# Kernel tuning notes

Measured on AMD Instinct MI355X. Metric: run time of the kernel, lower is better.

## Reference

```python
import jax, jax.numpy as jnp
import numpy as np
from jax.scipy.special import logsumexp

B, T, V, E, H, C, L = 128, 1024, 21, 32, 100, 20, 2


def setup_inputs() -> dict:
    key = jax.random.key(0)
    ks = jax.random.split(key, 32)
    def n(i, shape, scale=0.1):
        return (jax.random.normal(ks[i], shape) * scale).astype(jnp.float32)
    inp = {}
    inp["tokens"] = jax.random.randint(ks[0], (B, T), 0, V)
    inp["seq_lengths"] = jnp.full((B,), T, dtype=jnp.int32)
    inp["emb"] = n(1, (V, E), 1.0)
    idx = 2
    for l in range(L):
        din = E if l == 0 else 2 * H
        for sfx in ["", "_rev"]:
            inp[f"W_ih_l{l}{sfx}"] = n(idx, (4 * H, din)); idx += 1
            inp[f"W_hh_l{l}{sfx}"] = n(idx, (4 * H, H)); idx += 1
            inp[f"b_ih_l{l}{sfx}"] = n(idx, (4 * H,)); idx += 1
            inp[f"b_hh_l{l}{sfx}"] = n(idx, (4 * H,)); idx += 1
    inp["fW"] = n(idx, (C, 2 * H)); idx += 1
    inp["fb"] = n(idx, (C,)); idx += 1
    inp["gW"] = n(idx, (C * C, 2 * H)); idx += 1
    inp["gb"] = n(idx, (C * C,)); idx += 1
    inp["h0"] = n(idx, (2 * L, B, H), 1.0); idx += 1
    inp["c0"] = n(idx, (2 * L, B, H), 1.0)
    return inp


def _lstm_dir(x, Wih, Whh, bih, bhh, h0, c0, reverse):
    # x: [B,T,D]; precompute input projection once (PyTorch gate order i,f,g,o)
    xp = jnp.einsum('btd,gd->btg', x, Wih) + bih + bhh  # [B,T,4H]
    def step(carry, xt):
        h, c = carry
        gates = xt + h @ Whh.T
        i, f, g, o = jnp.split(gates, 4, axis=-1)
        c = jax.nn.sigmoid(f) * c + jax.nn.sigmoid(i) * jnp.tanh(g)
        h = jax.nn.sigmoid(o) * jnp.tanh(c)
        return (h, c), h
    _, hs = jax.lax.scan(step, (h0, c0), jnp.swapaxes(xp, 0, 1), reverse=reverse)
    return jnp.swapaxes(hs, 0, 1)  # [B,T,H]


def _crf_alpha(f, g):
    # alpha[0]=f[0]; alpha[t]=f[t]+LSE_i(alpha[t-1,i]+g[t,i,:])
    fs = jnp.swapaxes(f, 0, 1)  # [T,B,C]
    gs = jnp.swapaxes(g, 0, 1)  # [T,B,C,C]
    def step(a, fg):
        ft, gt = fg
        a = ft + logsumexp(a[:, :, None] + gt, axis=1)
        return a, a
    _, alphas = jax.lax.scan(step, fs[0], (fs[1:], gs[1:]))
    return jnp.swapaxes(jnp.concatenate([fs[:1], alphas], 0), 0, 1)


def _crf_beta(f, g):
    # beta[T-1]=0; beta[t]=LSE_j(g[t+1,:,j]+f[t+1,j]+beta[t+1,j])
    fs = jnp.swapaxes(f, 0, 1)
    gs = jnp.swapaxes(g, 0, 1)
    def step(b, fg):
        fnx, gnx = fg
        b = logsumexp(gnx + (fnx + b)[:, None, :], axis=2)
        return b, b
    bT = jnp.zeros_like(fs[0])
    _, betas = jax.lax.scan(step, bT, (fs[1:], gs[1:]), reverse=True)
    return jnp.swapaxes(jnp.concatenate([betas, bT[None]], 0), 0, 1)


def reference(tokens, seq_lengths, emb,
              W_ih_l0, W_hh_l0, b_ih_l0, b_hh_l0,
              W_ih_l0_rev, W_hh_l0_rev, b_ih_l0_rev, b_hh_l0_rev,
              W_ih_l1, W_hh_l1, b_ih_l1, b_hh_l1,
              W_ih_l1_rev, W_hh_l1_rev, b_ih_l1_rev, b_hh_l1_rev,
              fW, fb, gW, gb, h0, c0):
    x = emb[tokens]  # [B,T,E]
    # layer 0 (bidirectional)
    of = _lstm_dir(x, W_ih_l0, W_hh_l0, b_ih_l0, b_hh_l0, h0[0], c0[0], False)
    ob = _lstm_dir(x, W_ih_l0_rev, W_hh_l0_rev, b_ih_l0_rev, b_hh_l0_rev, h0[1], c0[1], True)
    x1 = jnp.concatenate([of, ob], axis=-1)  # dropout between layers: eval mode (identity)
    # layer 1
    of = _lstm_dir(x1, W_ih_l1, W_hh_l1, b_ih_l1, b_hh_l1, h0[2], c0[2], False)
    ob = _lstm_dir(x1, W_ih_l1_rev, W_hh_l1_rev, b_ih_l1_rev, b_hh_l1_rev, h0[3], c0[3], True)
    h = jnp.concatenate([of, ob], axis=-1)  # [B,T,2H]
    # pad_packed_sequence zeroes positions beyond seq_lengths
    mask = (jnp.arange(T)[None, :] < seq_lengths[:, None]).astype(h.dtype)
    h = h * mask[:, :, None]
    f_out = h @ fW.T + fb                      # [B,T,C] emissions
    g_out = (h @ gW.T + gb).reshape(B, T, C, C)  # [B,T,C,C] transitions
    alpha = _crf_alpha(f_out, g_out)
    beta = _crf_beta(f_out, g_out)
    logZ = logsumexp(alpha[:, -1], axis=-1)    # [B]
    log_marg = alpha + beta - logZ[:, None, None]
    return (jnp.exp(log_marg), f_out, g_out, alpha, beta)
```

## Files before the change

kernel.cpp:

```cpp
#include <hip/hip_runtime.h>
#include <hip/hip_bf16.h>

#define B_ 128
#define T_ 1024
#define E_ 32
#define H_ 100
#define C_ 20
#define M_ (B_*T_)

typedef __attribute__((ext_vector_type(8))) short bf16x8v;
typedef __attribute__((ext_vector_type(4))) float f32x4v;
typedef __attribute__((ext_vector_type(2))) _Float16 h2v;
typedef unsigned short u16;
typedef unsigned int u32;

static __device__ __forceinline__ short f2b(float x) {
  union { __hip_bfloat16 b; short s; } u;
  u.b = __float2bfloat16(x);
  return u.s;
}
static __device__ __forceinline__ float b2f(u16 x) {
  return __uint_as_float(((u32)x) << 16);
}

#if __has_builtin(__builtin_amdgcn_fdot2)
#define FDOT2(w, p, c) __builtin_amdgcn_fdot2((w), (p), (c), false)
#else
static __device__ __forceinline__ float FDOT2(h2v w, h2v p, float c) {
  return fmaf((float)w[1], (float)p[1], fmaf((float)w[0], (float)p[0], c));
}
#endif

__global__ void embed_k(const int* __restrict__ tok, const float* __restrict__ emb,
                        float* __restrict__ x0) {
  int idx = blockIdx.x * 256 + threadIdx.x;
  int bt = idx >> 5;
  int e  = idx & 31;
  x0[idx] = emb[tok[bt] * E_ + e];
}

template<int ABF, int OBF>
__global__ __launch_bounds__(256) void gemm_mfma_t(
    const void* __restrict__ Av, const float* __restrict__ W,
    const float* __restrict__ b1, const float* __restrict__ b2,
    void* __restrict__ Cv, int K, int N, int ldc)
{
  __shared__ short as[64 * 40];
  __shared__ short ws[64 * 40];
  const float* Af = (const float*)Av;
  const u16*   Ab = (const u16*)Av;
  float* Cf = (float*)Cv;
  u16*   Cb = (u16*)Cv;
  int tid = threadIdx.x, lane = tid & 63, w = tid >> 6;
  int lr = lane & 15, lq = lane >> 4;
  size_t m0 = (size_t)blockIdx.x * 64;
  int n0 = blockIdx.y * 64;
  int srow = tid >> 2;
  int sk = (tid & 3) * 8;
  bool wok = (n0 + srow) < N;
  const float* Wp = wok ? (W + (size_t)(n0 + srow) * K + sk) : W;
  size_t arow = (m0 + srow) * (size_t)K;
  f32x4v acc[4];
  #pragma unroll
  for (int r = 0; r < 4; ++r) acc[r] = (f32x4v){0.f, 0.f, 0.f, 0.f};
  int ksteps = (K + 31) / 32;
  for (int ks = 0; ks < ksteps; ++ks) {
    int kk = ks * 32;
    bf16x8v av, wv;
    if (kk + sk + 7 < K) {
      if (ABF) {
        av = *(const bf16x8v*)(Ab + arow + kk + sk);
      } else {
        float4 a0 = *(const float4*)(Af + arow + kk + sk);
        float4 a1 = *(const float4*)(Af + arow + kk + sk + 4);
        av[0]=f2b(a0.x); av[1]=f2b(a0.y); av[2]=f2b(a0.z); av[3]=f2b(a0.w);
        av[4]=f2b(a1.x); av[5]=f2b(a1.y); av[6]=f2b(a1.z); av[7]=f2b(a1.w);
      }
      if (wok) {
        float4 w0 = *(const float4*)(Wp + kk);
        float4 w1 = *(const float4*)(Wp + kk + 4);
        wv[0]=f2b(w0.x); wv[1]=f2b(w0.y); wv[2]=f2b(w0.z); wv[3]=f2b(w0.w);
        wv[4]=f2b(w1.x); wv[5]=f2b(w1.y); wv[6]=f2b(w1.z); wv[7]=f2b(w1.w);
      } else {
        #pragma unroll
        for (int j = 0; j < 8; ++j) wv[j] = 0;
      }
    } else {
      #pragma unroll
      for (int j = 0; j < 8; ++j) {
        int k = kk + sk + j;
        av[j] = (k < K) ? (ABF ? (short)Ab[arow + k] : f2b(Af[arow + k])) : (short)0;
        wv[j] = (wok && k < K) ? f2b(W[(size_t)(n0 + srow) * K + k]) : (short)0;
      }
    }
    *(bf16x8v*)&as[srow * 40 + sk] = av;
    *(bf16x8v*)&ws[srow * 40 + sk] = wv;
    __syncthreads();
    bf16x8v bf = *(const bf16x8v*)&ws[(16 * w + lr) * 40 + 8 * lq];
    #pragma unroll
    for (int r = 0; r < 4; ++r) {
      bf16x8v af = *(const bf16x8v*)&as[(16 * r + lr) * 40 + 8 * lq];
      acc[r] = __builtin_amdgcn_mfma_f32_16x16x32_bf16(af, bf, acc[r], 0, 0, 0);
    }
    __syncthreads();
  }
  int col = n0 + 16 * w + lr;
  if (col < N) {
    float bv = (b1 ? b1[col] : 0.f) + (b2 ? b2[col] : 0.f);
    #pragma unroll
    for (int r = 0; r < 4; ++r)
      #pragma unroll
      for (int rg = 0; rg < 4; ++rg) {
        size_t off = (m0 + 16 * r + 4 * lq + rg) * (size_t)ldc + col;
        float v = acc[r][rg] + bv;
        if (OBF) Cb[off] = (u16)f2b(v); else Cf[off] = v;
      }
  }
}

__global__ __launch_bounds__(256, 1) void lstm_scan(
    const u16* __restrict__ xp,
    const float* __restrict__ WhhF, const float* __restrict__ WhhR,
    const float* __restrict__ h0, const float* __restrict__ c0,
    const int* __restrict__ seqlen,
    u16* __restrict__ outbuf,
    int layer)
{
  int wg = blockIdx.x; int dir = wg & 1; int b = wg >> 1;
  int tid = threadIdx.x;
  const float* Whh = dir ? WhhR : WhhF;
  const u16* xpp = xp + ((size_t)dir * B_ + b) * T_ * 400;
  const float* h0p = h0 + ((size_t)(2 * layer + dir) * B_ + b) * H_;
  const float* c0p = c0 + ((size_t)(2 * layer + dir) * B_ + b) * H_;
  __shared__ __align__(16) float gsh[400];
  __shared__ __align__(16) _Float16 hph[112];
  bool act = (tid < 200);
  u32 w0p[52], w1p[52];
  if (act) {
    const float* r0 = Whh + (size_t)(2 * tid) * H_;
    const float* r1 = Whh + (size_t)(2 * tid + 1) * H_;
    #pragma unroll
    for (int j = 0; j < 52; ++j) {
      float a0 = (j < 50) ? r0[2 * j] : 0.f;
      float a1 = (j < 50) ? r0[2 * j + 1] : 0.f;
      float c0v = (j < 50) ? r1[2 * j] : 0.f;
      float c1v = (j < 50) ? r1[2 * j + 1] : 0.f;
      w0p[j] = __builtin_bit_cast(u32, (h2v){(_Float16)a0, (_Float16)a1});
      w1p[j] = __builtin_bit_cast(u32, (h2v){(_Float16)c0v, (_Float16)c1v});
    }
    #pragma unroll
    for (int j = 0; j < 52; ++j)
      asm volatile("" : "+v"(w0p[j]), "+v"(w1p[j]));
  }
  if (tid < 112) hph[tid] = (_Float16)((tid < H_) ? h0p[tid] : 0.f);
  float c = (tid < H_) ? c0p[tid] : 0.f;
  int sl = seqlen ? seqlen[b] : T_;
  __syncthreads();
  int tstep = dir ? -1 : 1;
  int t0 = dir ? (T_ - 1) : 0;
  ushort2 xc = make_ushort2(0, 0), xn = make_ushort2(0, 0);
  if (act) {
    xc = *(const ushort2*)(xpp + (size_t)t0 * 400 + 2 * tid);
    xn = *(const ushort2*)(xpp + (size_t)(t0 + tstep) * 400 + 2 * tid);
  }
  for (int tt = 0; tt < T_; ++tt) {
    int t = t0 + tstep * tt;
    ushort2 xn2 = make_ushort2(0, 0);
    if (act && tt + 2 < T_)
      xn2 = *(const ushort2*)(xpp + (size_t)(t + 2 * tstep) * 400 + 2 * tid);
    if (act) {
      float a0 = b2f(xc.x), a1 = b2f(xc.y);
      #pragma unroll
      for (int q = 0; q < 13; ++q) {
        f32x4v hp = ((const f32x4v*)hph)[q];
        #pragma unroll
        for (int i = 0; i < 4; ++i) {
          h2v p = __builtin_bit_cast(h2v, hp[i]);
          a0 = FDOT2(__builtin_bit_cast(h2v, w0p[4 * q + i]), p, a0);
          a1 = FDOT2(__builtin_bit_cast(h2v, w1p[4 * q + i]), p, a1);
        }
      }
      *(float2*)&gsh[2 * tid] = make_float2(a0, a1);
    }
    __syncthreads();
    if (tid < H_) {
      float gi = gsh[tid], gf = gsh[H_ + tid], gg = gsh[2 * H_ + tid], go = gsh[3 * H_ + tid];
      float si = 1.f / (1.f + __expf(-gi));
      float sf = 1.f / (1.f + __expf(-gf));
      float so = 1.f / (1.f + __expf(-go));
      float tg = 1.f - 2.f / (1.f + __expf(2.f * gg));
      c = fmaf(sf, c, si * tg);
      float tc = 1.f - 2.f / (1.f + __expf(2.f * c));
      float h = so * tc;
      hph[tid] = (_Float16)h;
      outbuf[((size_t)b * T_ + t) * 200 + dir * H_ + tid] = (t < sl) ? (u16)f2b(h) : (u16)0;
    }
    __syncthreads();
    xc = xn; xn = xn2;
  }
}

__global__ __launch_bounds__(64) void crf_k(
    const float* __restrict__ f, const float* __restrict__ g,
    float* __restrict__ alpha, float* __restrict__ beta)
{
  int wg = blockIdx.x;
  int lane = threadIdx.x;
  __shared__ __align__(16) float gl[4][400];
  __shared__ __align__(16) float aw[20];
  bool stv = lane < 50;
  int p0 = 8 * lane;
  float4 rA0, rA1, rB0, rB1;

  if (wg < B_) {
    int b = wg;
    const float* fp = f + (size_t)b * T_ * C_;
    const float* gp = g + (size_t)b * T_ * C_ * C_;
    float* ap = alpha + (size_t)b * T_ * C_;
    if (lane < C_) {
      float a0 = fp[lane];
      ap[lane] = a0;
      aw[lane] = a0;
    }
    if (stv) {
      float4 v0 = *(const float4*)(gp + 400 + p0);
      float4 v1 = *(const float4*)(gp + 404 + p0);
      *(float4*)&gl[1 & 3][p0] = v0;  *(float4*)&gl[1 & 3][p0 + 4] = v1;
      v0 = *(const float4*)(gp + 800 + p0);
      v1 = *(const float4*)(gp + 804 + p0);
      *(float4*)&gl[2 & 3][p0] = v0;  *(float4*)&gl[2 & 3][p0 + 4] = v1;
      rA0 = *(const float4*)(gp + 1200 + p0);
      rA1 = *(const float4*)(gp + 1204 + p0);
    }
    for (int t = 1; t < T_; ++t) {
      if (stv && (t + 3 < T_)) {
        rB0 = *(const float4*)(gp + (size_t)(t + 3) * 400 + p0);
        rB1 = *(const float4*)(gp + (size_t)(t + 3) * 400 + p0 + 4);
      }
      if (lane < C_) {
        const float* gr = &gl[t & 3][0];
        float ft = fp[(size_t)t * C_ + lane];
        float awv[20];
        #pragma unroll
        for (int q = 0; q < 5; ++q)
          *(f32x4v*)&awv[4 * q] = ((const f32x4v*)aw)[q];
        float s[20];
        #pragma unroll
        for (int i = 0; i < 20; ++i)
          s[i] = awv[i] + gr[i * 20 + lane];
        float m4[5];
        #pragma unroll
        for (int q = 0; q < 5; ++q)
          m4[q] = fmaxf(fmaxf(s[4*q], s[4*q+1]), fmaxf(s[4*q+2], s[4*q+3]));
        float m = fmaxf(fmaxf(m4[0], m4[1]), fmaxf(fmaxf(m4[2], m4[3]), m4[4]));
        float e4[5];
        #pragma unroll
        for (int q = 0; q < 5; ++q) {
          float e0 = __expf(s[4*q] - m),   e1 = __expf(s[4*q+1] - m);
          float e2 = __expf(s[4*q+2] - m), e3 = __expf(s[4*q+3] - m);
          e4[q] = (e0 + e1) + (e2 + e3);
        }
        float sum = (e4[0] + e4[1]) + ((e4[2] + e4[3]) + e4[4]);
        float an = ft + m + __logf(sum);
        ap[(size_t)t * C_ + lane] = an;
        aw[lane] = an;
      }
      if (stv && (t + 2 < T_)) {
        *(float4*)&gl[(t + 2) & 3][p0] = rA0;
        *(float4*)&gl[(t + 2) & 3][p0 + 4] = rA1;
      }
      rA0 = rB0; rA1 = rB1;
    }
  } else {
    int b = wg - B_;
    const float* fp = f + (size_t)b * T_ * C_;
    const float* gp = g + (size_t)b * T_ * C_ * C_;
    float* bp = beta + (size_t)b * T_ * C_;
    if (lane < C_) {
      bp[(size_t)(T_ - 1) * C_ + lane] = 0.f;
      aw[lane] = fp[(size_t)(T_ - 1) * C_ + lane];
    }
    if (stv) {
      float4 v0 = *(const float4*)(gp + (size_t)(T_ - 1) * 400 + p0);
      float4 v1 = *(const float4*)(gp + (size_t)(T_ - 1) * 400 + p0 + 4);
      *(float4*)&gl[(T_ - 1) & 3][p0] = v0;  *(float4*)&gl[(T_ - 1) & 3][p0 + 4] = v1;
      v0 = *(const float4*)(gp + (size_t)(T_ - 2) * 400 + p0);
      v1 = *(const float4*)(gp + (size_t)(T_ - 2) * 400 + p0 + 4);
      *(float4*)&gl[(T_ - 2) & 3][p0] = v0;  *(float4*)&gl[(T_ - 2) & 3][p0 + 4] = v1;
      rA0 = *(const float4*)(gp + (size_t)(T_ - 3) * 400 + p0);
      rA1 = *(const float4*)(gp + (size_t)(T_ - 3) * 400 + p0 + 4);
    }
    for (int u = 1; u < T_; ++u) {
      int t = T_ - 1 - u;
      int r = t + 1;
      if (stv && (r - 3 >= 1)) {
        rB0 = *(const float4*)(gp + (size_t)(r - 3) * 400 + p0);
        rB1 = *(const float4*)(gp + (size_t)(r - 3) * 400 + p0 + 4);
      }
      if (lane < C_) {
        const float* gr = &gl[r & 3][lane * 20];
        float fcur = fp[(size_t)t * C_ + lane];
        float awv[20];
        #pragma unroll
        for (int q = 0; q < 5; ++q)
          *(f32x4v*)&awv[4 * q] = ((const f32x4v*)aw)[q];
        float s[20];
        #pragma unroll
        for (int q = 0; q < 5; ++q) {
          f32x4v gq = *(const f32x4v*)&gr[4 * q];
          s[4*q]   = awv[4*q]   + gq[0];
          s[4*q+1] = awv[4*q+1] + gq[1];
          s[4*q+2] = awv[4*q+2] + gq[2];
          s[4*q+3] = awv[4*q+3] + gq[3];
        }
        float m4[5];
        #pragma unroll
        for (int q = 0; q < 5; ++q)
          m4[q] = fmaxf(fmaxf(s[4*q], s[4*q+1]), fmaxf(s[4*q+2], s[4*q+3]));
        float m = fmaxf(fmaxf(m4[0], m4[1]), fmaxf(fmaxf(m4[2], m4[3]), m4[4]));
        float e4[5];
        #pragma unroll
        for (int q = 0; q < 5; ++q) {
          float e0 = __expf(s[4*q] - m),   e1 = __expf(s[4*q+1] - m);
          float e2 = __expf(s[4*q+2] - m), e3 = __expf(s[4*q+3] - m);
          e4[q] = (e0 + e1) + (e2 + e3);
        }
        float sum = (e4[0] + e4[1]) + ((e4[2] + e4[3]) + e4[4]);
        float bn = m + __logf(sum);
        bp[(size_t)t * C_ + lane] = bn;
        aw[lane] = fcur + bn;
      }
      if (stv && (r - 2 >= 1)) {
        *(float4*)&gl[(r - 2) & 3][p0] = rA0;
        *(float4*)&gl[(r - 2) & 3][p0 + 4] = rA1;
      }
      rA0 = rB0; rA1 = rB1;
    }
  }
}

__global__ void logz_k(const float* __restrict__ alpha, float* __restrict__ lz) {
  int b = blockIdx.x; int lane = threadIdx.x;
  float a = (lane < C_) ? alpha[((size_t)b * T_ + (T_ - 1)) * C_ + lane] : -3.0e38f;
  float m = a;
  #pragma unroll
  for (int o = 32; o > 0; o >>= 1) m = fmaxf(m, __shfl_xor(m, o));
  float e = (lane < C_) ? __expf(a - m) : 0.f;
  #pragma unroll
  for (int o = 32; o > 0; o >>= 1) e += __shfl_xor(e, o);
  if (lane == 0) lz[b] = m + __logf(e);
}

__global__ void marg_k(const float* __restrict__ alpha, const float* __restrict__ beta,
                       const float* __restrict__ lz, float* __restrict__ out0) {
  size_t idx = (size_t)blockIdx.x * 256 + threadIdx.x;
  int b = (int)(idx / (T_ * C_));
  out0[idx] = __expf(alpha[idx] + beta[idx] - lz[b]);
}

extern "C" void kernel_launch(void* const* d_in, const int* in_sizes, int n_in,
                              void* d_out, int out_size, void* d_ws, size_t ws_size,
                              hipStream_t stream) {
  const int*   tok   = (const int*)d_in[0];
  const int*   seq   = (const int*)d_in[1];
  const float* emb   = (const float*)d_in[2];
  const float* Wih0  = (const float*)d_in[3];
  const float* Whh0  = (const float*)d_in[4];
  const float* bih0  = (const float*)d_in[5];
  const float* bhh0  = (const float*)d_in[6];
  const float* Wih0r = (const float*)d_in[7];
  const float* Whh0r = (const float*)d_in[8];
  const float* bih0r = (const float*)d_in[9];
  const float* bhh0r = (const float*)d_in[10];
  const float* Wih1  = (const float*)d_in[11];
  const float* Whh1  = (const float*)d_in[12];
  const float* bih1  = (const float*)d_in[13];
  const float* bhh1  = (const float*)d_in[14];
  const float* Wih1r = (const float*)d_in[15];
  const float* Whh1r = (const float*)d_in[16];
  const float* bih1r = (const float*)d_in[17];
  const float* bhh1r = (const float*)d_in[18];
  const float* fW    = (const float*)d_in[19];
  const float* fb    = (const float*)d_in[20];
  const float* gW    = (const float*)d_in[21];
  const float* gb    = (const float*)d_in[22];
  const float* h0    = (const float*)d_in[23];
  const float* c0    = (const float*)d_in[24];

  float* ws = (float*)d_ws;
  float* x0  = ws;
  u16*   xp  = (u16*)(ws + 4194304);
  u16*   x1  = (u16*)(ws + 109051904);
  float* lz  = ws + 135266304;

  float* out   = (float*)d_out;
  float* f_out = out + 2621440;
  float* g_out = out + 5242880;
  float* a_out = out + 57671680;
  float* b_out = out + 60293120;

  embed_k<<<16384, 256, 0, stream>>>(tok, emb, x0);

  dim3 g400(2048, 7), g20(2048, 1);
  gemm_mfma_t<0,1><<<g400, 256, 0, stream>>>(x0, Wih0,  bih0,  bhh0,  xp,                    32, 400, 400);
  gemm_mfma_t<0,1><<<g400, 256, 0, stream>>>(x0, Wih0r, bih0r, bhh0r, xp + (size_t)52428800, 32, 400, 400);
  lstm_scan<<<256, 256, 0, stream>>>(xp, Whh0, Whh0r, h0, c0, nullptr, x1, 0);
  gemm_mfma_t<1,1><<<g400, 256, 0, stream>>>(x1, Wih1,  bih1,  bhh1,  xp,                    200, 400, 400);
  gemm_mfma_t<1,1><<<g400, 256, 0, stream>>>(x1, Wih1r, bih1r, bhh1r, xp + (size_t)52428800, 200, 400, 400);
  lstm_scan<<<256, 256, 0, stream>>>(xp, Whh1, Whh1r, h0, c0, seq, x1, 1);
  gemm_mfma_t<1,0><<<g20,  256, 0, stream>>>(x1, fW, fb, nullptr, f_out, 200, 20,  20);
  gemm_mfma_t<1,0><<<g400, 256, 0, stream>>>(x1, gW, gb, nullptr, g_out, 200, 400, 400);
  crf_k<<<256, 64, 0, stream>>>(f_out, g_out, a_out, b_out);
  logz_k<<<128, 64, 0, stream>>>(a_out, lz);
  marg_k<<<10240, 256, 0, stream>>>(a_out, b_out, lz, out);
}
```

Before: 2.739 ms.

## Restructure LSTM scan: split-K over 4 lanes per hidden unit, one barrier per step

The recurrent LSTM kernel now assigns four lanes to each hidden unit. Each lane computes a quarter of the K dimension for all four gates, and the partials are reduced with cross-lane shuffles. Every lane then evaluates the gate nonlinearities itself, so the shared gate buffer and one of the two per-step barriers go away. The hidden state is double-buffered in LDS. This shortens the per-step serial dot-product chain and removes a sync, at the cost of a larger block (448 threads), redundant activation math across lanes, and shuffle overhead.

After: 2.850 ms. +4.1%, slower.

```diff
diff --git a/kernel.cpp b/kernel.cpp
--- a/kernel.cpp
+++ b/kernel.cpp
@@ -21,6 +21,9 @@
 }
 static __device__ __forceinline__ float b2f(u16 x) {
   return __uint_as_float(((u32)x) << 16);
+}
+static __device__ __forceinline__ u16 f2h(float x) {
+  return __builtin_bit_cast(u16, (_Float16)x);
 }
 
 #if __has_builtin(__builtin_amdgcn_fdot2)
@@ -118,7 +121,7 @@
   }
 }
 
-__global__ __launch_bounds__(256, 1) void lstm_scan(
+__global__ __launch_bounds__(448, 1) void lstm_scan(
     const u16* __restrict__ xp,
     const float* __restrict__ WhhF, const float* __restrict__ WhhR,
     const float* __restrict__ h0, const float* __restrict__ c0,
@@ -132,71 +135,87 @@
   const u16* xpp = xp + ((size_t)dir * B_ + b) * T_ * 400;
   const float* h0p = h0 + ((size_t)(2 * layer + dir) * B_ + b) * H_;
   const float* c0p = c0 + ((size_t)(2 * layer + dir) * B_ + b) * H_;
-  __shared__ __align__(16) float gsh[400];
-  __shared__ __align__(16) _Float16 hph[112];
-  bool act = (tid < 200);
-  u32 w0p[52], w1p[52];
+  __shared__ u32 hbuf[2][56];
+  bool act = (tid < 400);
+  int u = tid >> 2, j = tid & 3;
+  u32 wp0[13], wp1[13], wp2[13], wp3[13];
   if (act) {
-    const float* r0 = Whh + (size_t)(2 * tid) * H_;
-    const float* r1 = Whh + (size_t)(2 * tid + 1) * H_;
+    const float* r0 = Whh + (size_t)(0 * 100 + u) * H_;
+    const float* r1 = Whh + (size_t)(1 * 100 + u) * H_;
+    const float* r2 = Whh + (size_t)(2 * 100 + u) * H_;
+    const float* r3 = Whh + (size_t)(3 * 100 + u) * H_;
     #pragma unroll
-    for (int j = 0; j < 52; ++j) {
-      float a0 = (j < 50) ? r0[2 * j] : 0.f;
-      float a1 = (j < 50) ? r0[2 * j + 1] : 0.f;
-      float c0v = (j < 50) ? r1[2 * j] : 0.f;
-      float c1v = (j < 50) ? r1[2 * j + 1] : 0.f;
-      w0p[j] = __builtin_bit_cast(u32, (h2v){(_Float16)a0, (_Float16)a1});
-      w1p[j] = __builtin_bit_cast(u32, (h2v){(_Float16)c0v, (_Float16)c1v});
+    for (int m = 0; m < 13; ++m) {
+      int kp = 13 * j + m;
+      bool rl = kp < 50;
+      int k = 2 * kp;
+      #define PK(rp) __builtin_bit_cast(u32, (h2v){(_Float16)(rl ? rp[k] : 0.f), (_Float16)(rl ? rp[k + 1] : 0.f)})
+      wp0[m] = PK(r0); wp1[m] = PK(r1); wp2[m] = PK(r2); wp3[m] = PK(r3);
+      #undef PK
     }
     #pragma unroll
-    for (int j = 0; j < 52; ++j)
-      asm volatile("" : "+v"(w0p[j]), "+v"(w1p[j]));
-  }
-  if (tid < 112) hph[tid] = (_Float16)((tid < H_) ? h0p[tid] : 0.f);
-  float c = (tid < H_) ? c0p[tid] : 0.f;
+    for (int m = 0; m < 13; ++m)
+      asm volatile("" : "+v"(wp0[m]), "+v"(wp1[m]), "+v"(wp2[m]), "+v"(wp3[m]));
+  }
+  if (tid < 112) {
+    u16 hv = (tid < H_) ? f2h(h0p[tid]) : (u16)0;
+    ((u16*)&hbuf[0][0])[tid] = hv;
+    ((u16*)&hbuf[1][0])[tid] = (u16)0;
+  }
+  float c = act ? c0p[u] : 0.f;
   int sl = seqlen ? seqlen[b] : T_;
-  __syncthreads();
   int tstep = dir ? -1 : 1;
   int t0 = dir ? (T_ - 1) : 0;
-  ushort2 xc = make_ushort2(0, 0), xn = make_ushort2(0, 0);
+  const u16* xq = xpp + (size_t)t0 * 400 + 100 * j + u;
+  u16 xc = 0, xn = 0;
   if (act) {
-    xc = *(const ushort2*)(xpp + (size_t)t0 * 400 + 2 * tid);
-    xn = *(const ushort2*)(xpp + (size_t)(t0 + tstep) * 400 + 2 * tid);
-  }
+    xc = xq[0];
+    xn = xq[(ptrdiff_t)tstep * 400];
+  }
+  __syncthreads();
   for (int tt = 0; tt < T_; ++tt) {
     int t = t0 + tstep * tt;
-    ushort2 xn2 = make_ushort2(0, 0);
+    int cur = tt & 1, nxt = cur ^ 1;
+    u16 xn2 = 0;
     if (act && tt + 2 < T_)
-      xn2 = *(const ushort2*)(xpp + (size_t)(t + 2 * tstep) * 400 + 2 * tid);
+      xn2 = xq[(ptrdiff_t)(2 * tstep) * 400];
     if (act) {
-      float a0 = b2f(xc.x), a1 = b2f(xc.y);
+      u32 hp[13];
       #pragma unroll
-      for (int q = 0; q < 13; ++q) {
-        f32x4v hp = ((const f32x4v*)hph)[q];
-        #pragma unroll
-        for (int i = 0; i < 4; ++i) {
-          h2v p = __builtin_bit_cast(h2v, hp[i]);
-          a0 = FDOT2(__builtin_bit_cast(h2v, w0p[4 * q + i]), p, a0);
-          a1 = FDOT2(__builtin_bit_cast(h2v, w1p[4 * q + i]), p, a1);
-        }
-      }
-      *(float2*)&gsh[2 * tid] = make_float2(a0, a1);
-    }
-    __syncthreads();
-    if (tid < H_) {
-      float gi = gsh[tid], gf = gsh[H_ + tid], gg = gsh[2 * H_ + tid], go = gsh[3 * H_ + tid];
-      float si = 1.f / (1.f + __expf(-gi));
-      float sf = 1.f / (1.f + __expf(-gf));
-      float so = 1.f / (1.f + __expf(-go));
-      float tg = 1.f - 2.f / (1.f + __expf(2.f * gg));
+      for (int m = 0; m < 13; ++m) hp[m] = hbuf[cur][13 * j + m];
+      float a0 = 0.f, a1 = 0.f, a2 = 0.f, a3 = 0.f;
+      #pragma unroll
+      for (int m = 0; m < 13; ++m) {
+        h2v p = __builtin_bit_cast(h2v, hp[m]);
+        a0 = FDOT2(__builtin_bit_cast(h2v, wp0[m]), p, a0);
+        a1 = FDOT2(__builtin_bit_cast(h2v, wp1[m]), p, a1);
+        a2 = FDOT2(__builtin_bit_cast(h2v, wp2[m]), p, a2);
+        a3 = FDOT2(__builtin_bit_cast(h2v, wp3[m]), p, a3);
+      }
+      float xval = b2f(xc);
+      a0 += (j == 0) ? xval : 0.f;
+      a1 += (j == 1) ? xval : 0.f;
+      a2 += (j == 2) ? xval : 0.f;
+      a3 += (j == 3) ? xval : 0.f;
+      a0 += __shfl_xor(a0, 1); a0 += __shfl_xor(a0, 2);
+      a1 += __shfl_xor(a1, 1); a1 += __shfl_xor(a1, 2);
+      a2 += __shfl_xor(a2, 1); a2 += __shfl_xor(a2, 2);
+      a3 += __shfl_xor(a3, 1); a3 += __shfl_xor(a3, 2);
+      float si = 1.f / (1.f + __expf(-a0));
+      float sf = 1.f / (1.f + __expf(-a1));
+      float tg = 1.f - 2.f / (1.f + __expf(2.f * a2));
+      float so = 1.f / (1.f + __expf(-a3));
       c = fmaf(sf, c, si * tg);
       float tc = 1.f - 2.f / (1.f + __expf(2.f * c));
       float h = so * tc;
-      hph[tid] = (_Float16)h;
-      outbuf[((size_t)b * T_ + t) * 200 + dir * H_ + tid] = (t < sl) ? (u16)f2b(h) : (u16)0;
+      if (j == 0) {
+        ((u16*)&hbuf[nxt][0])[u] = f2h(h);
+        outbuf[((size_t)b * T_ + t) * 200 + dir * H_ + u] = (t < sl) ? (u16)f2b(h) : (u16)0;
+      }
+      xc = xn; xn = xn2;
+      xq += (ptrdiff_t)tstep * 400;
     }
     __syncthreads();
-    xc = xn; xn = xn2;
   }
 }
 
@@ -404,10 +423,10 @@
   dim3 g400(2048, 7), g20(2048, 1);
   gemm_mfma_t<0,1><<<g400, 256, 0, stream>>>(x0, Wih0,  bih0,  bhh0,  xp,                    32, 400, 400);
   gemm_mfma_t<0,1><<<g400, 256, 0, stream>>>(x0, Wih0r, bih0r, bhh0r, xp + (size_t)52428800, 32, 400, 400);
-  lstm_scan<<<256, 256, 0, stream>>>(xp, Whh0, Whh0r, h0, c0, nullptr, x1, 0);
+  lstm_scan<<<256, 448, 0, stream>>>(xp, Whh0, Whh0r, h0, c0, nullptr, x1, 0);
   gemm_mfma_t<1,1><<<g400, 256, 0, stream>>>(x1, Wih1,  bih1,  bhh1,  xp,                    200, 400, 400);
   gemm_mfma_t<1,1><<<g400, 256, 0, stream>>>(x1, Wih1r, bih1r, bhh1r, xp + (size_t)52428800, 200, 400, 400);
-  lstm_scan<<<256, 256, 0, stream>>>(xp, Whh1, Whh1r, h0, c0, seq, x1, 1);
+  lstm_scan<<<256, 448, 0, stream>>>(xp, Whh1, Whh1r, h0, c0, seq, x1, 1);
   gemm_mfma_t<1,0><<<g20,  256, 0, stream>>>(x1, fW, fb, nullptr, f_out, 200, 20,  20);
   gemm_mfma_t<1,0><<<g400, 256, 0, stream>>>(x1, gW, gb, nullptr, g_out, 200, 400, 400);
   crf_k<<<256, 64, 0, stream>>>(f_out, g_out, a_out, b_out);
```
